# Kernel optimization log

Measured on AMD Instinct MI355X. Metric: run time of the kernel, lower is better.

## Reference

```python
import jax, jax.numpy as jnp
import numpy as np

NHEAD = 8

def layernorm(x, g, b, eps=1e-5):
    mu = x.mean(-1, keepdims=True)
    var = ((x - mu) ** 2).mean(-1, keepdims=True)
    return (x - mu) / jnp.sqrt(var + eps) * g + b

def linear_attention(q, k, v, eps=1e-6):
    # LoFTR kernelized linear attention: phi(x) = elu(x) + 1
    Q = jax.nn.elu(q) + 1.0          # [n, l, h, d]
    K = jax.nn.elu(k) + 1.0          # [n, s, h, d]
    s_len = v.shape[1]
    KV = jnp.einsum("nshd,nshv->nhdv", K, v / s_len)
    Z = 1.0 / (jnp.einsum("nlhd,nhd->nlh", Q, K.sum(axis=1)) + eps)
    return jnp.einsum("nlhd,nhdv,nlh->nlhv", Q, KV, Z) * s_len

def _block(x_base, q, k, v, Wm, W1, W2, g1, b1, g2, b2):
    bs, L, h, dh = q.shape
    msg = linear_attention(q, k, v).reshape(bs, L, h * dh)
    msg = layernorm(msg @ Wm, g1, b1)
    hcat = jnp.concatenate([x_base, msg], axis=2)          # [bs, L, 2*d]
    out = jax.nn.relu(hcat @ W1) @ W2
    return layernorm(out, g2, b2)

def setup_inputs() -> dict:
    key = jax.random.key(0)
    ks = jax.random.split(key, 8)
    bs, L, S, d = 8, 4800, 4800, 256
    w = lambda k, i, o: jax.random.normal(k, (i, o), jnp.float32) * 0.02
    return {
        "x": jax.random.normal(ks[0], (bs, L, d), jnp.float32),
        "source": jax.random.normal(ks[1], (bs, S, d), jnp.float32),
        "Wq": w(ks[2], d, d), "Wk": w(ks[3], d, d), "Wv": w(ks[4], d, d),
        "Wm": w(ks[5], d, d),
        "W1": w(ks[6], 2 * d, 2 * d), "W2": w(ks[7], 2 * d, d),
        "g1": jnp.ones((d,), jnp.float32), "b1": jnp.zeros((d,), jnp.float32),
        "g2": jnp.ones((d,), jnp.float32), "b2": jnp.zeros((d,), jnp.float32),
    }

def reference(x, source, Wq, Wk, Wv, Wm, W1, W2, g1, b1, g2, b2):
    bs, L, d = x.shape
    h = NHEAD
    dh = d // h
    q = (x @ Wq).reshape(bs, L, h, dh)
    k = (source @ Wk).reshape(bs, -1, h, dh)
    v = (source @ Wv).reshape(bs, -1, h, dh)
    # permute-then-view reinterpretations, exactly as in the torch code
    p13 = lambda t: t.transpose(0, 1, 3, 2).reshape(bs, -1, h, dh)  # permute(0,1,3,2)
    p21 = lambda t: t.transpose(0, 2, 1, 3).reshape(bs, -1, h, dh)  # permute(0,2,1,3)
    p32 = lambda t: t.transpose(0, 3, 2, 1).reshape(bs, -1, h, dh)  # permute(0,3,2,1)
    blk = lambda xb, qq, kk, vv: _block(xb, qq, kk, vv, Wm, W1, W2, g1, b1, g2, b2)
    m = blk(x, q, k, v)
    m3 = blk(x, p13(q), p13(k), p13(v))
    x_mid = x + 0.5 * (m + m3)
    m1 = blk(x_mid, p21(q), p21(k), p21(v))
    m2 = blk(x_mid, p32(q), p32(k), p32(v))
    return x_mid + 0.5 * (m1 + m2)
```

## Files before the change

kernel.cpp:

```cpp
#include <hip/hip_runtime.h>
#include <type_traits>
#include <cstdint>
#include <cstddef>

#define L_SEQ 4800
#define DMODEL 256
#define BS 8
#define MROWS (BS*L_SEQ)
#define PERBATCH (L_SEQ*DMODEL)
#define KVSET 67584

typedef __attribute__((ext_vector_type(8))) short bfrag8;
typedef __attribute__((ext_vector_type(4))) float floatx4;

__device__ __forceinline__ float bf2f(unsigned short u){
  union { unsigned int i; float f; } x; x.i = ((unsigned int)u) << 16; return x.f;
}
__device__ __forceinline__ unsigned short f2bf(float f){
  union { float f; unsigned int i; } x; x.f = f;
  x.i += 0x7fff + ((x.i >> 16) & 1);
  return (unsigned short)(x.i >> 16);
}
__device__ __forceinline__ float phi(float x){
  return x > 0.f ? x + 1.f : __expf(x);
}
__device__ __forceinline__ void gll16(const void* g, void* l){
  __builtin_amdgcn_global_load_lds((const __attribute__((address_space(1))) unsigned int*)g,
      (__attribute__((address_space(3))) unsigned int*)l, 16, 0, 0);
}

template<typename TC, bool RELU>
__global__ __launch_bounds__(256) void gemm_mfma(const unsigned short* __restrict__ A,
                                                 const unsigned short* __restrict__ Bt,
                                                 TC* __restrict__ C, int M, int N, int K){
  __shared__ unsigned short Al[2][4096];
  __shared__ unsigned short Bl[2][4096];
  const int tid  = threadIdx.x;
  const int lane = tid & 63;
  const int wave = tid >> 6;
  const int row0 = blockIdx.y << 7;
  const int col0 = blockIdx.x << 7;
  const int wr0  = (wave & 1) << 6;
  const int wc0  = (wave >> 1) << 6;
  const int m = lane & 15, q = lane >> 4;
  const int sw = (m >> 1) & 3;

  floatx4 acc[4][4] = {};

  const int u0 = tid, u1 = tid + 256;
  const int r0 = u0 >> 2, s0 = u0 & 3;
  const int r1 = u1 >> 2, s1 = u1 & 3;

  auto stage = [&](int k0, int b){
    gll16(A  + (size_t)(row0 + r0)*K + k0 + ((s0 ^ ((r0 >> 1) & 3)) << 3), Al[b] + (size_t)u0*8);
    gll16(A  + (size_t)(row0 + r1)*K + k0 + ((s1 ^ ((r1 >> 1) & 3)) << 3), Al[b] + (size_t)u1*8);
    gll16(Bt + (size_t)(col0 + r0)*K + k0 + ((s0 ^ ((r0 >> 1) & 3)) << 3), Bl[b] + (size_t)u0*8);
    gll16(Bt + (size_t)(col0 + r1)*K + k0 + ((s1 ^ ((r1 >> 1) & 3)) << 3), Bl[b] + (size_t)u1*8);
  };

  stage(0, 0);
  const int nk = K >> 5;
  for (int ks = 0; ks < nk; ks++){
    asm volatile("s_waitcnt vmcnt(0) lgkmcnt(0)" ::: "memory");
    __builtin_amdgcn_s_barrier();
    asm volatile("" ::: "memory");
    if (ks < nk - 1) stage((ks + 1) << 5, (ks + 1) & 1);
    const unsigned short* ab = Al[ks & 1];
    const unsigned short* bb = Bl[ks & 1];
    bfrag8 af[4], bf[4];
    #pragma unroll
    for (int t = 0; t < 4; t++){
      af[t] = *(const bfrag8*)(ab + (size_t)(wr0 + t*16 + m)*32 + ((q ^ sw) << 3));
      bf[t] = *(const bfrag8*)(bb + (size_t)(wc0 + t*16 + m)*32 + ((q ^ sw) << 3));
    }
    #pragma unroll
    for (int mt = 0; mt < 4; mt++)
      #pragma unroll
      for (int nt = 0; nt < 4; nt++)
        acc[mt][nt] = __builtin_amdgcn_mfma_f32_16x16x32_bf16(af[mt], bf[nt], acc[mt][nt], 0, 0, 0);
  }

  #pragma unroll
  for (int mt = 0; mt < 4; mt++){
    #pragma unroll
    for (int nt = 0; nt < 4; nt++){
      const int col  = col0 + wc0 + nt*16 + m;
      const int rowb = row0 + wr0 + mt*16 + q*4;
      #pragma unroll
      for (int i = 0; i < 4; i++){
        float v = acc[mt][nt][i];
        if (RELU) v = v > 0.f ? v : 0.f;
        if constexpr (std::is_same<TC,float>::value) C[(size_t)(rowb+i)*N + col] = v;
        else                                         C[(size_t)(rowb+i)*N + col] = f2bf(v);
      }
    }
  }
}

__global__ __launch_bounds__(256) void gemm_w1(const unsigned short* __restrict__ Axc,
                                               const unsigned short* __restrict__ Amsg,
                                               const unsigned short* __restrict__ Bt,
                                               unsigned short* __restrict__ C){
  __shared__ unsigned short Al[2][4096];
  __shared__ unsigned short Bl[2][4096];
  const int tid  = threadIdx.x;
  const int lane = tid & 63;
  const int wave = tid >> 6;
  const int row0 = blockIdx.y << 7;
  const int col0 = blockIdx.x << 7;
  const int wr0  = (wave & 1) << 6;
  const int wc0  = (wave >> 1) << 6;
  const int m = lane & 15, q = lane >> 4;
  const int sw = (m >> 1) & 3;
  const int K = 512;

  floatx4 acc[4][4] = {};

  const int u0 = tid, u1 = tid + 256;
  const int r0 = u0 >> 2, s0 = u0 & 3;
  const int r1 = u1 >> 2, s1 = u1 & 3;

  auto stage = [&](int ks, int b){
    const int k0 = ks << 5;
    const unsigned short* As = (ks < 8) ? Axc : Amsg;
    const int kk = k0 & 255;
    gll16(As + (size_t)(row0 + r0)*256 + kk + ((s0 ^ ((r0 >> 1) & 3)) << 3), Al[b] + (size_t)u0*8);
    gll16(As + (size_t)(row0 + r1)*256 + kk + ((s1 ^ ((r1 >> 1) & 3)) << 3), Al[b] + (size_t)u1*8);
    gll16(Bt + (size_t)(col0 + r0)*K + k0 + ((s0 ^ ((r0 >> 1) & 3)) << 3), Bl[b] + (size_t)u0*8);
    gll16(Bt + (size_t)(col0 + r1)*K + k0 + ((s1 ^ ((r1 >> 1) & 3)) << 3), Bl[b] + (size_t)u1*8);
  };

  stage(0, 0);
  for (int ks = 0; ks < 16; ks++){
    asm volatile("s_waitcnt vmcnt(0) lgkmcnt(0)" ::: "memory");
    __builtin_amdgcn_s_barrier();
    asm volatile("" ::: "memory");
    if (ks < 15) stage(ks + 1, (ks + 1) & 1);
    const unsigned short* ab = Al[ks & 1];
    const unsigned short* bb = Bl[ks & 1];
    bfrag8 af[4], bf[4];
    #pragma unroll
    for (int t = 0; t < 4; t++){
      af[t] = *(const bfrag8*)(ab + (size_t)(wr0 + t*16 + m)*32 + ((q ^ sw) << 3));
      bf[t] = *(const bfrag8*)(bb + (size_t)(wc0 + t*16 + m)*32 + ((q ^ sw) << 3));
    }
    #pragma unroll
    for (int mt = 0; mt < 4; mt++)
      #pragma unroll
      for (int nt = 0; nt < 4; nt++)
        acc[mt][nt] = __builtin_amdgcn_mfma_f32_16x16x32_bf16(af[mt], bf[nt], acc[mt][nt], 0, 0, 0);
  }

  #pragma unroll
  for (int mt = 0; mt < 4; mt++){
    #pragma unroll
    for (int nt = 0; nt < 4; nt++){
      const int col  = col0 + wc0 + nt*16 + m;
      const int rowb = row0 + wr0 + mt*16 + q*4;
      #pragma unroll
      for (int i = 0; i < 4; i++){
        float v = acc[mt][nt][i];
        v = v > 0.f ? v : 0.f;
        C[(size_t)(rowb+i)*512 + col] = f2bf(v);
      }
    }
  }
}

template<int MODE>
__global__ __launch_bounds__(256) void gemm_lnv2(const unsigned short* __restrict__ A0,
                                                 const unsigned short* __restrict__ A1,
                                                 const unsigned short* __restrict__ Bt,
                                                 const float* __restrict__ g,
                                                 const float* __restrict__ b,
                                                 unsigned short* __restrict__ ob0,
                                                 unsigned short* __restrict__ ob1,
                                                 float* __restrict__ of,
                                                 int K, int add){
  __shared__ unsigned short Ab[4096];
  __shared__ unsigned short Bb[16384];
  __shared__ float2 LNp[64][4];
  __shared__ float2 LNmu[64];
  const int tid = threadIdx.x;
  const int wv = tid >> 6, lane = tid & 63;
  const int m = lane & 15, qd = lane >> 4;
  const int sw = (m >> 1) & 3;
  const int row0 = blockIdx.x << 6;
  const unsigned short* A = (MODE == 0 && blockIdx.y) ? A1 : A0;
  unsigned short* ob = (MODE == 0 && blockIdx.y) ? ob1 : ob0;

  floatx4 acc[4][4] = {};
  const int nsteps = K >> 6;
  for (int o = 0; o < nsteps; o++){
    const int k0 = o << 6;
    #pragma unroll
    for (int i = 0; i < 2; i++){
      int u = (i << 8) + tid;
      int r = (u & 255) >> 2, s = u & 3, h = u >> 8;
      gll16(A + (size_t)(row0 + r)*K + k0 + h*32 + ((s ^ ((r >> 1) & 3)) << 3),
            Ab + (size_t)u*8);
    }
    #pragma unroll
    for (int i = 0; i < 8; i++){
      int u = (i << 8) + tid;
      int c = (u & 1023) >> 2, s = u & 3, h = u >> 10;
      gll16(Bt + (size_t)c*K + k0 + h*32 + ((s ^ ((c >> 1) & 3)) << 3),
            Bb + (size_t)u*8);
    }
    asm volatile("s_waitcnt vmcnt(0)" ::: "memory");
    __syncthreads();
    #pragma unroll
    for (int j = 0; j < 2; j++){
      bfrag8 af[4], bf[4];
      #pragma unroll
      for (int mt = 0; mt < 4; mt++){
        int r = mt*16 + m;
        af[mt] = *(const bfrag8*)(Ab + (size_t)j*2048 + (size_t)r*32 + ((qd ^ sw) << 3));
      }
      #pragma unroll
      for (int nt = 0; nt < 4; nt++){
        int c = wv*64 + nt*16 + m;
        bf[nt] = *(const bfrag8*)(Bb + (size_t)j*8192 + (size_t)c*32 + ((qd ^ sw) << 3));
      }
      #pragma unroll
      for (int mt = 0; mt < 4; mt++)
        #pragma unroll
        for (int nt = 0; nt < 4; nt++)
          acc[mt][nt] = __builtin_amdgcn_mfma_f32_16x16x32_bf16(af[mt], bf[nt], acc[mt][nt], 0, 0, 0);
    }
    __syncthreads();
  }

  #pragma unroll
  for (int mt = 0; mt < 4; mt++)
    #pragma unroll
    for (int i = 0; i < 4; i++){
      float s = 0.f, q = 0.f;
      #pragma unroll
      for (int nt = 0; nt < 4; nt++){ float v = acc[mt][nt][i]; s += v; q += v*v; }
      #pragma unroll
      for (int o = 1; o < 16; o <<= 1){ s += __shfl_xor(s, o, 64); q += __shfl_xor(q, o, 64); }
      if (m == 0) LNp[mt*16 + qd*4 + i][wv] = make_float2(s, q);
    }
  __syncthreads();
  if (tid < 64){
    float2 p0 = LNp[tid][0], p1 = LNp[tid][1], p2 = LNp[tid][2], p3 = LNp[tid][3];
    float S = p0.x + p1.x + p2.x + p3.x;
    float Q = p0.y + p1.y + p2.y + p3.y;
    float mean = S * (1.f/256.f);
    float var  = Q * (1.f/256.f) - mean*mean;
    LNmu[tid] = make_float2(mean, rsqrtf(var + 1e-5f));
  }
  __syncthreads();

  float gv[4], bv[4];
  #pragma unroll
  for (int nt = 0; nt < 4; nt++){ int col = wv*64 + nt*16 + m; gv[nt] = g[col]; bv[nt] = b[col]; }
  #pragma unroll
  for (int mt = 0; mt < 4; mt++)
    #pragma unroll
    for (int i = 0; i < 4; i++){
      int row = mt*16 + qd*4 + i;
      float2 ms = LNmu[row];
      const size_t rowg = row0 + row;
      #pragma unroll
      for (int nt = 0; nt < 4; nt++){
        int col = wv*64 + nt*16 + m;
        float y = (acc[mt][nt][i] - ms.x) * ms.y * gv[nt] + bv[nt];
        if constexpr (MODE == 0){
          ob[rowg*256 + col] = f2bf(y);
        } else {
          float* p = of + rowg*256 + col;
          if (add) y += *p;
          *p = y;
        }
      }
    }
}

__global__ __launch_bounds__(256) void wconv(const float* __restrict__ W, unsigned short* __restrict__ Wt,
                                             int kshift, int N){
  int idx = blockIdx.x*256 + threadIdx.x;
  int kk = idx & ((1 << kshift) - 1);
  int nn = idx >> kshift;
  Wt[idx] = f2bf(W[(size_t)kk*N + nn]);
}
__global__ __launch_bounds__(256) void conv_bf16(const float* __restrict__ in, unsigned short* __restrict__ out){
  int i = blockIdx.x*256 + threadIdx.x;
  float4 v = ((const float4*)in)[i];
  ushort4 o; o.x = f2bf(v.x); o.y = f2bf(v.y); o.z = f2bf(v.z); o.w = f2bf(v.w);
  ((ushort4*)out)[i] = o;
}

__global__ __launch_bounds__(256) void permute1(const unsigned short* __restrict__ sA, unsigned short* __restrict__ dA,
                                                const unsigned short* __restrict__ sB, unsigned short* __restrict__ dB){
  const unsigned short* s = blockIdx.z ? sB : sA;
  unsigned short*       d = blockIdx.z ? dB : dA;
  __shared__ unsigned short tile[1024];
  const int t = threadIdx.x;
  const size_t base = (size_t)blockIdx.x * 1024;
  #pragma unroll
  for (int i = 0; i < 4; i++) tile[i*256 + t] = s[base + i*256 + t];
  __syncthreads();
  const int pg = ((t & 7) << 5) + (t >> 3);
  #pragma unroll
  for (int i = 0; i < 4; i++) d[base + i*256 + t] = tile[i*256 + pg];
}

__global__ __launch_bounds__(256) void permute2(const unsigned short* __restrict__ sA, unsigned short* __restrict__ dA,
                                                const unsigned short* __restrict__ sB, unsigned short* __restrict__ dB){
  const unsigned short* s = blockIdx.z ? sB : sA;
  unsigned short*       d = blockIdx.z ? dB : dA;
  __shared__ unsigned short tile[64*256];
  const int t = threadIdx.x;
  const int rr0 = blockIdx.x * 64;
  const size_t boff = (size_t)blockIdx.y * PERBATCH;
  #pragma unroll
  for (int i = 0; i < 16; i++){
    int u = i*256 + t;
    *(ushort4*)&tile[u*4] = *(const ushort4*)&s[boff + (size_t)rr0*256 + (size_t)u*4];
  }
  __syncthreads();
  #pragma unroll
  for (int i = 0; i < 8; i++){
    #pragma unroll
    for (int w = 0; w < 2; w++){
      int u = w*256 + t;
      int rr = u >> 3, c4 = (u & 7) << 2;
      ushort4 v = *(const ushort4*)&tile[rr*256 + i*32 + c4];
      *(ushort4*)&d[boff + (size_t)i*153600 + (size_t)rr0*32 + (size_t)u*4] = v;
    }
  }
}

__global__ __launch_bounds__(256) void permute3(const unsigned short* __restrict__ sA, unsigned short* __restrict__ dA,
                                                const unsigned short* __restrict__ sB, unsigned short* __restrict__ dB){
  const unsigned short* s = blockIdx.z ? sB : sA;
  unsigned short*       d = blockIdx.z ? dB : dA;
  __shared__ unsigned short tile[64*258];
  const int t = threadIdx.x;
  const int ll0 = blockIdx.x * 64;
  const size_t boff = (size_t)blockIdx.y * PERBATCH;
  #pragma unroll
  for (int i = 0; i < 32; i++){
    int u = i*256 + t;
    int row = u >> 7, col = (u & 127) << 1;
    *(ushort2*)&tile[row*258 + col] = *(const ushort2*)&s[boff + (size_t)(ll0+row)*256 + col];
  }
  __syncthreads();
  const int cw = t >> 6;
  const int ll = t & 63;
  #pragma unroll
  for (int cc = 0; cc < 256; cc += 4){
    int c = cc + cw;
    int sigma = ((c & 31) << 3) + (c >> 5);
    d[boff + (size_t)sigma*4800 + ll0 + ll] = tile[ll*258 + c];
  }
}

__global__ __launch_bounds__(256) void attn_stats(const unsigned short* __restrict__ kq,
                                                  const unsigned short* __restrict__ vq,
                                                  float* __restrict__ KV, float* __restrict__ Ksum){
  const int chunk = blockIdx.x, h = blockIdx.y, n = blockIdx.z;
  const int t = threadIdx.x;
  const int d = t >> 3;
  const int w4 = (t & 7) << 2;
  const size_t boff = (size_t)n * PERBATCH;
  __shared__ float kb[8][32], vb[8][32];
  const int lr = t >> 5, lj = t & 31;
  float a0=0.f, a1=0.f, a2=0.f, a3=0.f, ks=0.f;
  const int s0 = chunk * 240;
  for (int s = s0; s < s0 + 240; s += 8){
    int srci = (s + lr)*256 + (h << 5) + lj;
    kb[lr][lj] = phi(bf2f(kq[boff + srci]));
    vb[lr][lj] = bf2f(vq[boff + srci]);
    __syncthreads();
    #pragma unroll
    for (int r = 0; r < 8; r++){
      float kd = kb[r][d];
      ks += kd;
      a0 += kd * vb[r][w4+0];
      a1 += kd * vb[r][w4+1];
      a2 += kd * vb[r][w4+2];
      a3 += kd * vb[r][w4+3];
    }
    __syncthreads();
  }
  float* kvp = KV + (size_t)((((n<<3)+h)<<5) + d)*32 + w4;
  atomicAdd(kvp+0, a0);
  atomicAdd(kvp+1, a1);
  atomicAdd(kvp+2, a2);
  atomicAdd(kvp+3, a3);
  if ((t & 7) == 0) atomicAdd(Ksum + (((n<<3)+h)<<5) + d, ks);
}

__global__ __launch_bounds__(256) void attn_apply(const unsigned short* __restrict__ qq,
                                                  const float* __restrict__ KV,
                                                  const float* __restrict__ Ksum,
                                                  unsigned short* __restrict__ msg){
  __shared__ float kvs[8192];
  __shared__ float kss[256];
  __shared__ float Qs[4096];
  const int t = threadIdx.x;
  const int n = blockIdx.y;
  const int row0 = blockIdx.x << 4;
  const size_t boff = (size_t)n * PERBATCH;

  #pragma unroll
  for (int i = 0; i < 32; i++) kvs[i*256 + t] = KV[(size_t)n*8192 + i*256 + t];
  kss[t] = Ksum[n*256 + t];
  #pragma unroll
  for (int r = 0; r < 16; r++)
    Qs[r*256 + t] = phi(bf2f(qq[boff + (size_t)(row0 + r)*256 + t]));
  __syncthreads();

  const int h = t >> 5, w = t & 31;
  const float* kvh = kvs + h*1024;
  const float* ksh = kss + h*32;
  float acc[16], den[16];
  #pragma unroll
  for (int r = 0; r < 16; r++){ acc[r] = 0.f; den[r] = 1e-6f; }

  #pragma unroll
  for (int d4 = 0; d4 < 8; d4++){
    const float k0 = kvh[(d4*4+0)*32 + w];
    const float k1 = kvh[(d4*4+1)*32 + w];
    const float k2 = kvh[(d4*4+2)*32 + w];
    const float k3 = kvh[(d4*4+3)*32 + w];
    const float s0 = ksh[d4*4+0], s1 = ksh[d4*4+1], s2 = ksh[d4*4+2], s3 = ksh[d4*4+3];
    #pragma unroll
    for (int r = 0; r < 16; r++){
      float4 qv = *(const float4*)&Qs[r*256 + h*32 + d4*4];
      acc[r] += qv.x*k0 + qv.y*k1 + qv.z*k2 + qv.w*k3;
      den[r] += qv.x*s0 + qv.y*s1 + qv.z*s2 + qv.w*s3;
    }
  }
  #pragma unroll
  for (int r = 0; r < 16; r++)
    msg[boff + (size_t)(row0 + r)*256 + t] = f2bf(acc[r]/den[r]);
}

__global__ __launch_bounds__(256) void xmid_k(const float* __restrict__ x, const float* __restrict__ macc,
                                              float* __restrict__ xmid, unsigned short* __restrict__ xcbf){
  size_t i = (size_t)blockIdx.x*256 + threadIdx.x;
  float v = x[i] + 0.5f*macc[i];
  xmid[i] = v;
  xcbf[i] = f2bf(v);
}
__global__ __launch_bounds__(256) void final_k(float* __restrict__ out, const float* __restrict__ macc){
  size_t i = (size_t)blockIdx.x*256 + threadIdx.x;
  out[i] = out[i] + 0.5f*macc[i];
}
__global__ __launch_bounds__(256) void zero_k(float* __restrict__ p, int n){
  int i = blockIdx.x*256 + threadIdx.x;
  if (i < n) p[i] = 0.f;
}

extern "C" void kernel_launch(void* const* d_in, const int* in_sizes, int n_in,
                              void* d_out, int out_size, void* d_ws, size_t ws_size,
                              hipStream_t stream){
  const float* x   = (const float*)d_in[0];
  const float* src = (const float*)d_in[1];
  const float* Wq  = (const float*)d_in[2];
  const float* Wk  = (const float*)d_in[3];
  const float* Wv  = (const float*)d_in[4];
  const float* Wm  = (const float*)d_in[5];
  const float* W1  = (const float*)d_in[6];
  const float* W2  = (const float*)d_in[7];
  const float* g1  = (const float*)d_in[8];
  const float* b1  = (const float*)d_in[9];
  const float* g2  = (const float*)d_in[10];
  const float* b2  = (const float*)d_in[11];
  float* out = (float*)d_out;

  char* ws = (char*)d_ws;
  size_t off = 0;
  auto alloc = [&](size_t bytes) -> void* {
    void* p = ws + off;
    off += (bytes + 255) & ~(size_t)255;
    return p;
  };
  unsigned short* qB   = (unsigned short*)alloc((size_t)MROWS*256*2);
  unsigned short* kB   = (unsigned short*)alloc((size_t)MROWS*256*2);
  unsigned short* vB   = (unsigned short*)alloc((size_t)MROWS*256*2);
  unsigned short* mlnB = (unsigned short*)alloc((size_t)MROWS*512*2);
  float* t1   = (float*)alloc((size_t)MROWS*256*4);
  float* macc = (float*)alloc((size_t)MROWS*256*4);
  float* KV4  = (float*)alloc((size_t)4*KVSET*4);
  unsigned short* WqT = (unsigned short*)alloc((size_t)256*256*2);
  unsigned short* WkT = (unsigned short*)alloc((size_t)256*256*2);
  unsigned short* WvT = (unsigned short*)alloc((size_t)256*256*2);
  unsigned short* WmT = (unsigned short*)alloc((size_t)256*256*2);
  unsigned short* W1T = (unsigned short*)alloc((size_t)512*512*2);
  unsigned short* W2T = (unsigned short*)alloc((size_t)256*512*2);
  (void)ws_size; (void)in_sizes; (void)n_in; (void)out_size;

  unsigned short* srcbf  = (unsigned short*)t1;
  unsigned short* xcbf   = srcbf + (size_t)MROWS*256;
  unsigned short* qP     = (unsigned short*)t1;
  unsigned short* msgln0 = mlnB;
  unsigned short* msgln1 = mlnB + (size_t)MROWS*256;
  unsigned short* hid    = kB;
  float* xmid = out;

  const dim3 blk(256);

  wconv<<<dim3(256),  blk, 0, stream>>>(Wq, WqT, 8, 256);
  wconv<<<dim3(256),  blk, 0, stream>>>(Wk, WkT, 8, 256);
  wconv<<<dim3(256),  blk, 0, stream>>>(Wv, WvT, 8, 256);
  wconv<<<dim3(256),  blk, 0, stream>>>(Wm, WmT, 8, 256);
  wconv<<<dim3(1024), blk, 0, stream>>>(W1, W1T, 9, 512);
  wconv<<<dim3(512),  blk, 0, stream>>>(W2, W2T, 9, 256);
  conv_bf16<<<dim3(9600), blk, 0, stream>>>(src, srcbf);
  conv_bf16<<<dim3(9600), blk, 0, stream>>>(x,   xcbf);

  gemm_mfma<unsigned short, false><<<dim3(2,300), blk, 0, stream>>>(xcbf,  WqT, qB, MROWS, 256, 256);
  gemm_mfma<unsigned short, false><<<dim3(2,300), blk, 0, stream>>>(srcbf, WkT, kB, MROWS, 256, 256);
  gemm_mfma<unsigned short, false><<<dim3(2,300), blk, 0, stream>>>(srcbf, WvT, vB, MROWS, 256, 256);

  unsigned short* kP = (unsigned short*)macc;
  unsigned short* vP = kP + (size_t)MROWS*256;
  zero_k<<<dim3(1056), blk, 0, stream>>>(KV4, 4*KVSET);
  attn_stats<<<dim3(20,8,8), blk, 0, stream>>>(kB, vB, KV4 + 0*KVSET, KV4 + 0*KVSET + 65536);
  permute1<<<dim3(9600,1,2), blk, 0, stream>>>(kB, kP, vB, vP);
  attn_stats<<<dim3(20,8,8), blk, 0, stream>>>(kP, vP, KV4 + 1*KVSET, KV4 + 1*KVSET + 65536);
  permute2<<<dim3(75,8,2),  blk, 0, stream>>>(kB, kP, vB, vP);
  attn_stats<<<dim3(20,8,8), blk, 0, stream>>>(kP, vP, KV4 + 2*KVSET, KV4 + 2*KVSET + 65536);
  permute3<<<dim3(75,8,2),  blk, 0, stream>>>(kB, kP, vB, vP);
  attn_stats<<<dim3(20,8,8), blk, 0, stream>>>(kP, vP, KV4 + 3*KVSET, KV4 + 3*KVSET + 65536);

  auto run_pair = [&](int modeA, int modeB, int addA){
    {
      const float* KV   = KV4 + (size_t)modeA*KVSET;
      const unsigned short* qsrc = qB;
      if (modeA == 2){ permute2<<<dim3(75,8,1), blk, 0, stream>>>(qB, qP, nullptr, nullptr); qsrc = qP; }
      attn_apply<<<dim3(300,BS), blk, 0, stream>>>(qsrc, KV, KV + 65536, kB);
    }
    {
      const float* KV   = KV4 + (size_t)modeB*KVSET;
      if (modeB == 1)      permute1<<<dim3(9600,1,1), blk, 0, stream>>>(qB, qP, nullptr, nullptr);
      else                 permute3<<<dim3(75,8,1),   blk, 0, stream>>>(qB, qP, nullptr, nullptr);
      attn_apply<<<dim3(300,BS), blk, 0, stream>>>(qP, KV, KV + 65536, vB);
    }
    gemm_lnv2<0><<<dim3(600,2), blk, 0, stream>>>(kB, vB, WmT, g1, b1, msgln0, msgln1, nullptr, 256, 0);
    gemm_w1<<<dim3(4,300), blk, 0, stream>>>(xcbf, msgln0, W1T, hid);
    gemm_lnv2<1><<<dim3(600,1), blk, 0, stream>>>(hid, nullptr, W2T, g2, b2, nullptr, nullptr, macc, 512, addA);
    gemm_w1<<<dim3(4,300), blk, 0, stream>>>(xcbf, msgln1, W1T, hid);
    gemm_lnv2<1><<<dim3(600,1), blk, 0, stream>>>(hid, nullptr, W2T, g2, b2, nullptr, nullptr, macc, 512, 1);
  };

  run_pair(0, 1, 0);
  xmid_k<<<dim3(MROWS), blk, 0, stream>>>(x, macc, xmid, xcbf);
  run_pair(2, 3, 0);
  final_k<<<dim3(MROWS), blk, 0, stream>>>(out, macc);
}
```

Measured before the change: 979.9 us.

## Unify W1/Wm/W2 GEMMs into 512-thread 128x256-tile kernel with double buffering

```diff
diff --git a/kernel.cpp b/kernel.cpp
--- a/kernel.cpp
+++ b/kernel.cpp
@@ -97,45 +97,61 @@
   }
 }
 
-__global__ __launch_bounds__(256) void gemm_w1(const unsigned short* __restrict__ Axc,
-                                               const unsigned short* __restrict__ Amsg,
-                                               const unsigned short* __restrict__ Bt,
-                                               unsigned short* __restrict__ C){
+template<int MODE, int NK>
+__global__ __launch_bounds__(512) void gemm3(const unsigned short* __restrict__ A0,
+                                             const unsigned short* __restrict__ A1,
+                                             const unsigned short* __restrict__ Bt,
+                                             const float* __restrict__ g,
+                                             const float* __restrict__ b,
+                                             unsigned short* __restrict__ ob0,
+                                             unsigned short* __restrict__ ob1,
+                                             float* __restrict__ of,
+                                             int add){
   __shared__ unsigned short Al[2][4096];
-  __shared__ unsigned short Bl[2][4096];
+  __shared__ unsigned short Bl[2][8192];
+  __shared__ float2 LNp[128][4];
+  __shared__ float2 LNmu[128];
   const int tid  = threadIdx.x;
   const int lane = tid & 63;
   const int wave = tid >> 6;
   const int row0 = blockIdx.y << 7;
-  const int col0 = blockIdx.x << 7;
+  const int col0 = (MODE == 2) ? (blockIdx.x << 8) : 0;
   const int wr0  = (wave & 1) << 6;
   const int wc0  = (wave >> 1) << 6;
   const int m = lane & 15, q = lane >> 4;
   const int sw = (m >> 1) & 3;
-  const int K = 512;
+  constexpr int AST = (MODE == 1) ? 512 : 256;
+  constexpr int BST = (MODE == 0) ? 256 : 512;
+
+  const unsigned short* Asel = (MODE == 0 && blockIdx.z) ? A1 : A0;
+  unsigned short* ob = (MODE == 0 && blockIdx.z) ? ob1 : ob0;
+
+  const int ra = tid >> 2, sa = tid & 3;
+
+  auto stage = [&](int ks, int bsel){
+    const int k0 = ks << 5;
+    const unsigned short* As;
+    int aoff;
+    if constexpr (MODE == 2){ As = (ks < 8) ? A0 : A1; aoff = k0 & 255; }
+    else                    { As = Asel;               aoff = k0; }
+    gll16(As + (size_t)(row0 + ra)*AST + aoff + ((sa ^ ((ra >> 1) & 3)) << 3),
+          Al[bsel] + (size_t)tid*8);
+    #pragma unroll
+    for (int i = 0; i < 2; i++){
+      int u = (i << 9) + tid;
+      int c = u >> 2, sc = u & 3;
+      gll16(Bt + (size_t)(col0 + c)*BST + k0 + ((sc ^ ((c >> 1) & 3)) << 3),
+            Bl[bsel] + (size_t)u*8);
+    }
+  };
 
   floatx4 acc[4][4] = {};
-
-  const int u0 = tid, u1 = tid + 256;
-  const int r0 = u0 >> 2, s0 = u0 & 3;
-  const int r1 = u1 >> 2, s1 = u1 & 3;
-
-  auto stage = [&](int ks, int b){
-    const int k0 = ks << 5;
-    const unsigned short* As = (ks < 8) ? Axc : Amsg;
-    const int kk = k0 & 255;
-    gll16(As + (size_t)(row0 + r0)*256 + kk + ((s0 ^ ((r0 >> 1) & 3)) << 3), Al[b] + (size_t)u0*8);
-    gll16(As + (size_t)(row0 + r1)*256 + kk + ((s1 ^ ((r1 >> 1) & 3)) << 3), Al[b] + (size_t)u1*8);
-    gll16(Bt + (size_t)(col0 + r0)*K + k0 + ((s0 ^ ((r0 >> 1) & 3)) << 3), Bl[b] + (size_t)u0*8);
-    gll16(Bt + (size_t)(col0 + r1)*K + k0 + ((s1 ^ ((r1 >> 1) & 3)) << 3), Bl[b] + (size_t)u1*8);
-  };
-
   stage(0, 0);
-  for (int ks = 0; ks < 16; ks++){
+  for (int ks = 0; ks < NK; ks++){
     asm volatile("s_waitcnt vmcnt(0) lgkmcnt(0)" ::: "memory");
     __builtin_amdgcn_s_barrier();
     asm volatile("" ::: "memory");
-    if (ks < 15) stage(ks + 1, (ks + 1) & 1);
+    if (ks < NK - 1) stage(ks + 1, (ks + 1) & 1);
     const unsigned short* ab = Al[ks & 1];
     const unsigned short* bb = Bl[ks & 1];
     bfrag8 af[4], bf[4];
@@ -151,131 +167,73 @@
         acc[mt][nt] = __builtin_amdgcn_mfma_f32_16x16x32_bf16(af[mt], bf[nt], acc[mt][nt], 0, 0, 0);
   }
 
-  #pragma unroll
-  for (int mt = 0; mt < 4; mt++){
-    #pragma unroll
-    for (int nt = 0; nt < 4; nt++){
-      const int col  = col0 + wc0 + nt*16 + m;
-      const int rowb = row0 + wr0 + mt*16 + q*4;
+  if constexpr (MODE == 2){
+    #pragma unroll
+    for (int mt = 0; mt < 4; mt++){
+      #pragma unroll
+      for (int nt = 0; nt < 4; nt++){
+        const int col  = col0 + wc0 + nt*16 + m;
+        const int rowb = row0 + wr0 + mt*16 + q*4;
+        #pragma unroll
+        for (int i = 0; i < 4; i++){
+          float v = acc[mt][nt][i];
+          v = v > 0.f ? v : 0.f;
+          ob[(size_t)(rowb+i)*512 + col] = f2bf(v);
+        }
+      }
+    }
+  } else {
+    const int cg = wave >> 1;
+    #pragma unroll
+    for (int mt = 0; mt < 4; mt++)
       #pragma unroll
       for (int i = 0; i < 4; i++){
-        float v = acc[mt][nt][i];
-        v = v > 0.f ? v : 0.f;
-        C[(size_t)(rowb+i)*512 + col] = f2bf(v);
-      }
-    }
-  }
-}
-
-template<int MODE>
-__global__ __launch_bounds__(256) void gemm_lnv2(const unsigned short* __restrict__ A0,
-                                                 const unsigned short* __restrict__ A1,
-                                                 const unsigned short* __restrict__ Bt,
-                                                 const float* __restrict__ g,
-                                                 const float* __restrict__ b,
-                                                 unsigned short* __restrict__ ob0,
-                                                 unsigned short* __restrict__ ob1,
-                                                 float* __restrict__ of,
-                                                 int K, int add){
-  __shared__ unsigned short Ab[4096];
-  __shared__ unsigned short Bb[16384];
-  __shared__ float2 LNp[64][4];
-  __shared__ float2 LNmu[64];
-  const int tid = threadIdx.x;
-  const int wv = tid >> 6, lane = tid & 63;
-  const int m = lane & 15, qd = lane >> 4;
-  const int sw = (m >> 1) & 3;
-  const int row0 = blockIdx.x << 6;
-  const unsigned short* A = (MODE == 0 && blockIdx.y) ? A1 : A0;
-  unsigned short* ob = (MODE == 0 && blockIdx.y) ? ob1 : ob0;
-
-  floatx4 acc[4][4] = {};
-  const int nsteps = K >> 6;
-  for (int o = 0; o < nsteps; o++){
-    const int k0 = o << 6;
-    #pragma unroll
-    for (int i = 0; i < 2; i++){
-      int u = (i << 8) + tid;
-      int r = (u & 255) >> 2, s = u & 3, h = u >> 8;
-      gll16(A + (size_t)(row0 + r)*K + k0 + h*32 + ((s ^ ((r >> 1) & 3)) << 3),
-            Ab + (size_t)u*8);
-    }
-    #pragma unroll
-    for (int i = 0; i < 8; i++){
-      int u = (i << 8) + tid;
-      int c = (u & 1023) >> 2, s = u & 3, h = u >> 10;
-      gll16(Bt + (size_t)c*K + k0 + h*32 + ((s ^ ((c >> 1) & 3)) << 3),
-            Bb + (size_t)u*8);
-    }
-    asm volatile("s_waitcnt vmcnt(0)" ::: "memory");
-    __syncthreads();
-    #pragma unroll
-    for (int j = 0; j < 2; j++){
-      bfrag8 af[4], bf[4];
-      #pragma unroll
-      for (int mt = 0; mt < 4; mt++){
-        int r = mt*16 + m;
-        af[mt] = *(const bfrag8*)(Ab + (size_t)j*2048 + (size_t)r*32 + ((qd ^ sw) << 3));
-      }
-      #pragma unroll
-      for (int nt = 0; nt < 4; nt++){
-        int c = wv*64 + nt*16 + m;
-        bf[nt] = *(const bfrag8*)(Bb + (size_t)j*8192 + (size_t)c*32 + ((qd ^ sw) << 3));
-      }
-      #pragma unroll
-      for (int mt = 0; mt < 4; mt++)
+        float s = 0.f, qq = 0.f;
         #pragma unroll
-        for (int nt = 0; nt < 4; nt++)
-          acc[mt][nt] = __builtin_amdgcn_mfma_f32_16x16x32_bf16(af[mt], bf[nt], acc[mt][nt], 0, 0, 0);
-    }
-    __syncthreads();
-  }
-
-  #pragma unroll
-  for (int mt = 0; mt < 4; mt++)
-    #pragma unroll
-    for (int i = 0; i < 4; i++){
-      float s = 0.f, q = 0.f;
-      #pragma unroll
-      for (int nt = 0; nt < 4; nt++){ float v = acc[mt][nt][i]; s += v; q += v*v; }
-      #pragma unroll
-      for (int o = 1; o < 16; o <<= 1){ s += __shfl_xor(s, o, 64); q += __shfl_xor(q, o, 64); }
-      if (m == 0) LNp[mt*16 + qd*4 + i][wv] = make_float2(s, q);
-    }
-  __syncthreads();
-  if (tid < 64){
-    float2 p0 = LNp[tid][0], p1 = LNp[tid][1], p2 = LNp[tid][2], p3 = LNp[tid][3];
-    float S = p0.x + p1.x + p2.x + p3.x;
-    float Q = p0.y + p1.y + p2.y + p3.y;
-    float mean = S * (1.f/256.f);
-    float var  = Q * (1.f/256.f) - mean*mean;
-    LNmu[tid] = make_float2(mean, rsqrtf(var + 1e-5f));
-  }
-  __syncthreads();
-
-  float gv[4], bv[4];
-  #pragma unroll
-  for (int nt = 0; nt < 4; nt++){ int col = wv*64 + nt*16 + m; gv[nt] = g[col]; bv[nt] = b[col]; }
-  #pragma unroll
-  for (int mt = 0; mt < 4; mt++)
-    #pragma unroll
-    for (int i = 0; i < 4; i++){
-      int row = mt*16 + qd*4 + i;
-      float2 ms = LNmu[row];
-      const size_t rowg = row0 + row;
-      #pragma unroll
-      for (int nt = 0; nt < 4; nt++){
-        int col = wv*64 + nt*16 + m;
-        float y = (acc[mt][nt][i] - ms.x) * ms.y * gv[nt] + bv[nt];
-        if constexpr (MODE == 0){
-          ob[rowg*256 + col] = f2bf(y);
-        } else {
-          float* p = of + rowg*256 + col;
-          if (add) y += *p;
-          *p = y;
+        for (int nt = 0; nt < 4; nt++){ float v = acc[mt][nt][i]; s += v; qq += v*v; }
+        #pragma unroll
+        for (int o = 1; o < 16; o <<= 1){ s += __shfl_xor(s, o, 64); qq += __shfl_xor(qq, o, 64); }
+        if (m == 0){
+          int row = wr0 + mt*16 + q*4 + i;
+          float2* p = &LNp[row][cg];
+          *p = make_float2(s, qq);
         }
       }
-    }
+    __syncthreads();
+    if (tid < 128){
+      float2 p0 = LNp[tid][0], p1 = LNp[tid][1], p2 = LNp[tid][2], p3 = LNp[tid][3];
+      float S = p0.x + p1.x + p2.x + p3.x;
+      float Q = p0.y + p1.y + p2.y + p3.y;
+      float mean = S * (1.f/256.f);
+      float var  = Q * (1.f/256.f) - mean*mean;
+      LNmu[tid] = make_float2(mean, rsqrtf(var + 1e-5f));
+    }
+    __syncthreads();
+
+    float gv[4], bv[4];
+    #pragma unroll
+    for (int nt = 0; nt < 4; nt++){ int col = wc0 + nt*16 + m; gv[nt] = g[col]; bv[nt] = b[col]; }
+    #pragma unroll
+    for (int mt = 0; mt < 4; mt++)
+      #pragma unroll
+      for (int i = 0; i < 4; i++){
+        int row = wr0 + mt*16 + q*4 + i;
+        float2 ms = LNmu[row];
+        const size_t rowg = row0 + row;
+        #pragma unroll
+        for (int nt = 0; nt < 4; nt++){
+          int col = wc0 + nt*16 + m;
+          float y = (acc[mt][nt][i] - ms.x) * ms.y * gv[nt] + bv[nt];
+          if constexpr (MODE == 0){
+            ob[rowg*256 + col] = f2bf(y);
+          } else {
+            float* p = of + rowg*256 + col;
+            if (add) y += *p;
+            *p = y;
+          }
+        }
+      }
+  }
 }
 
 __global__ __launch_bounds__(256) void wconv(const float* __restrict__ W, unsigned short* __restrict__ Wt,
@@ -504,6 +462,7 @@
   float* xmid = out;
 
   const dim3 blk(256);
+  const dim3 blk512(512);
 
   wconv<<<dim3(256),  blk, 0, stream>>>(Wq, WqT, 8, 256);
   wconv<<<dim3(256),  blk, 0, stream>>>(Wk, WkT, 8, 256);
@@ -542,11 +501,11 @@
       else                 permute3<<<dim3(75,8,1),   blk, 0, stream>>>(qB, qP, nullptr, nullptr);
       attn_apply<<<dim3(300,BS), blk, 0, stream>>>(qP, KV, KV + 65536, vB);
     }
-    gemm_lnv2<0><<<dim3(600,2), blk, 0, stream>>>(kB, vB, WmT, g1, b1, msgln0, msgln1, nullptr, 256, 0);
-    gemm_w1<<<dim3(4,300), blk, 0, stream>>>(xcbf, msgln0, W1T, hid);
-    gemm_lnv2<1><<<dim3(600,1), blk, 0, stream>>>(hid, nullptr, W2T, g2, b2, nullptr, nullptr, macc, 512, addA);
-    gemm_w1<<<dim3(4,300), blk, 0, stream>>>(xcbf, msgln1, W1T, hid);
-    gemm_lnv2<1><<<dim3(600,1), blk, 0, stream>>>(hid, nullptr, W2T, g2, b2, nullptr, nullptr, macc, 512, 1);
+    gemm3<0,8><<<dim3(1,300,2), blk512, 0, stream>>>(kB, vB, WmT, g1, b1, msgln0, msgln1, nullptr, 0);
+    gemm3<2,16><<<dim3(2,300), blk512, 0, stream>>>(xcbf, msgln0, W1T, nullptr, nullptr, hid, nullptr, nullptr, 0);
+    gemm3<1,16><<<dim3(1,300), blk512, 0, stream>>>(hid, nullptr, W2T, g2, b2, nullptr, nullptr, macc, addA);
+    gemm3<2,16><<<dim3(2,300), blk512, 0, stream>>>(xcbf, msgln1, W1T, nullptr, nullptr, hid, nullptr, nullptr, 0);
+    gemm3<1,16><<<dim3(1,300), blk512, 0, stream>>>(hid, nullptr, W2T, g2, b2, nullptr, nullptr, macc, 1);
   };
 
   run_pair(0, 1, 0);
```

Result: slower. 1.019 ms (+4.0%).
